# Optimization experiments

Hardware: AMD Instinct MI355X
Metric: run time of the kernel (lower is better)

Reference implementation:

```python
import jax, jax.numpy as jnp
import numpy as np

NQ = 14            # n_qubits
NB = 2             # n_blocks
KLOC = 4           # k_local
K = 2 ** KLOC      # Hermitian observable dim = 16
NOFF = K * (K - 1) // 2   # 120 off-diagonal params
DEPTH = 3          # vqc_depth
IN_DIM = 784
OUT_DIM = 10
BATCH = 128
GROUPS = [list(range(s, s + KLOC)) for s in range(NQ - KLOC + 1)]  # sliding k-local groups
NOBS = len(GROUPS)  # 11
TOTAL_ENC = NB * ((NQ // 2) + ((NQ - 1) // 2)) * 15  # 390 SU(4) encoding params

# 15 two-qubit Pauli words in PennyLane's lexicographic IXYZ order (identity excluded)
_I = np.eye(2, dtype=np.complex64)
_X = np.array([[0, 1], [1, 0]], np.complex64)
_Y = np.array([[0, -1j], [1j, 0]], np.complex64)
_Z = np.array([[1, 0], [0, -1]], np.complex64)
_P = {'I': _I, 'X': _X, 'Y': _Y, 'Z': _Z}
_WORDS = [a + b for a in 'IXYZ' for b in 'IXYZ'][1:]
P15 = jnp.asarray(np.stack([np.kron(_P[w[0]], _P[w[1]]) for w in _WORDS]))  # (15,4,4)
CNOT = jnp.asarray(np.array([[1, 0, 0, 0], [0, 1, 0, 0], [0, 0, 0, 1], [0, 0, 1, 0]], np.complex64))
_ROWS, _COLS = np.tril_indices(K, -1)  # row-major lower-tri order == create_Hermitian fill order


def su4(theta):
    """PennyLane SpecialUnitary: U = expm(i * sum_m theta_m P_m), theta: (B,15).
    The generator is Hermitian, so use eigh instead of generic expm."""
    Hm = jnp.einsum('bm,mij->bij', theta.astype(jnp.complex64), P15)  # (B,4,4) Hermitian
    w, V = jnp.linalg.eigh(Hm)
    return jnp.einsum('bij,bj,bkj->bik', V, jnp.exp(1j * w.astype(jnp.complex64)), V.conj())


def apply_gate(state, U, wires):
    """Apply a k-qubit gate U ((B,2^k,2^k) or (2^k,2^k)) to state (B, 2,...,2)."""
    n = state.ndim - 1
    k = len(wires)
    axes = [w + 1 for w in wires]
    perm = [0] + axes + [a for a in range(1, n + 1) if a not in axes]
    st = jnp.transpose(state, perm)
    shp = st.shape
    st = st.reshape(shp[0], 2 ** k, -1)
    if U.ndim == 3:
        st = jnp.einsum('bij,bjr->bir', U, st)
    else:
        st = jnp.einsum('ij,bjr->bir', U, st)
    return jnp.transpose(st.reshape(shp), np.argsort(perm))


def expval_herm(state, H, wires):
    """<psi| H_{wires} |psi> per batch element."""
    n = state.ndim - 1
    axes = [w + 1 for w in wires]
    perm = [0] + axes + [a for a in range(1, n + 1) if a not in axes]
    st = jnp.transpose(state, perm).reshape(state.shape[0], H.shape[0], -1)
    return jnp.einsum('bkr,kl,blr->b', st.conj(), H, st).real


def create_hermitian(A, Bp, D):
    """Faithful port of create_Hermitian: lower-tri A+iB (row-major), diag D[1:] on
    positions 0..K-2 (D[0] unused, last diag 0), then H = h + h^dagger (diag doubled)."""
    h = jnp.zeros((K, K), jnp.complex64).at[_ROWS, _COLS].set(A + 1j * Bp)
    d = jnp.zeros((K,), A.dtype).at[jnp.arange(K - 1)].set(D[1:])
    h = h + jnp.diag(d).astype(jnp.complex64)
    return h + h.conj().T


def ry_mat(theta):
    c = jnp.cos(theta / 2)
    s = jnp.sin(theta / 2)
    return jnp.stack([jnp.stack([c, -s]), jnp.stack([s, c])]).astype(jnp.complex64)


def setup_inputs():
    key = jax.random.key(0)
    ks = jax.random.split(key, 9)
    lim = 1.0 / np.sqrt(IN_DIM)
    lim_h = 1.0 / np.sqrt(NOBS)
    return {
        'x': jax.random.normal(ks[0], (BATCH, IN_DIM), jnp.float32),
        'W_enc': jax.random.uniform(ks[1], (TOTAL_ENC, IN_DIM), jnp.float32, -lim, lim),
        'b_enc': jax.random.uniform(ks[2], (TOTAL_ENC,), jnp.float32, -lim, lim),
        'var_params': 0.01 * jax.random.normal(ks[3], (DEPTH, NQ), jnp.float32),
        'A': 2.0 * jax.random.normal(ks[4], (NOBS, NOFF), jnp.float32),
        'Bp': 2.0 * jax.random.normal(ks[5], (NOBS, NOFF), jnp.float32),
        'D': 2.0 * jax.random.normal(ks[6], (NOBS, K), jnp.float32),
        'W_head': jax.random.uniform(ks[7], (OUT_DIM, NOBS), jnp.float32, -lim_h, lim_h),
        'b_head': jax.random.uniform(ks[8], (OUT_DIM,), jnp.float32, -lim_h, lim_h),
    }


def reference(x, W_enc, b_enc, var_params, A, Bp, D, W_head, b_head):
    encoded = x @ W_enc.T + b_enc                      # (B, 390)
    Hs = jax.vmap(create_hermitian)(A, Bp, D)          # (NOBS, K, K)
    Bsz = x.shape[0]
    state = jnp.zeros((Bsz,) + (2,) * NQ, jnp.complex64).at[(slice(None),) + (0,) * NQ].set(1.0)
    # SU(4) brick-layer encoding: even pairs then odd pairs per block
    idx = 0
    for _ in range(NB):
        for q in list(range(0, NQ - 1, 2)) + list(range(1, NQ - 1, 2)):
            state = apply_gate(state, su4(encoded[:, idx:idx + 15]), [q, q + 1])
            idx += 15
    # variational RY + CNOT brick layers
    for layer in range(DEPTH):
        for q in range(NQ):
            state = apply_gate(state, ry_mat(var_params[layer, q]), [q])
        for q in list(range(0, NQ - 1, 2)) + list(range(1, NQ - 1, 2)):
            state = apply_gate(state, CNOT, [q, q + 1])
    q_out = jnp.stack([expval_herm(state, Hs[w], GROUPS[w]) for w in range(NOBS)], axis=1)
    q_out = q_out.astype(jnp.float32)                  # (B, NOBS)
    return q_out @ W_head.T + b_head                   # (B, OUT_DIM)
```

## Files before the change

### kernel.cpp

```cpp
#include <hip/hip_runtime.h>
#include <math.h>

#define NQ      14
#define NSTATE  16384
#define BATCH   128
#define DEPTH   3
#define NOBS    11
#define KDIM    16
#define NOFF    120
#define INDIM   784
#define OUTDIM  10

__device__ __forceinline__ int F2(int a) { return a + (a >> 4); }
#define PHYS2 (NSTATE + (NSTATE >> 4))

__device__ __forceinline__ float sbc(float x) {
  return __int_as_float(__builtin_amdgcn_readfirstlane(__float_as_int(x)));
}

__global__ __launch_bounds__(256) void enc_kernel(
    const float* __restrict__ x, const float* __restrict__ W,
    const float* __restrict__ bvec, float* __restrict__ theta)
{
  int wave = ((blockIdx.x << 2) | (threadIdx.x >> 6));
  int lane = threadIdx.x & 63;
  int g = wave >> 7;
  int b = wave & 127;

  const float4* x4 = (const float4*)(x + (size_t)b * INDIM);
  const float4* w4 = (const float4*)(W + (size_t)g * 15 * INDIM);

  float acc[15];
#pragma unroll
  for (int m = 0; m < 15; ++m) acc[m] = 0.f;
#pragma unroll
  for (int it = 0; it < 4; ++it) {
    int j4 = lane + it * 64;
    if (j4 < 196) {
      float4 xv = x4[j4];
#pragma unroll
      for (int m = 0; m < 15; ++m) {
        float4 wv = w4[m * 196 + j4];
        acc[m] = fmaf(xv.x, wv.x, fmaf(xv.y, wv.y, fmaf(xv.z, wv.z, fmaf(xv.w, wv.w, acc[m]))));
      }
    }
  }
#pragma unroll
  for (int m = 0; m < 15; ++m) {
#pragma unroll
    for (int off = 32; off; off >>= 1) acc[m] += __shfl_xor(acc[m], off);
  }
  if (lane == 0) {
#pragma unroll
    for (int m = 0; m < 15; ++m) theta[(size_t)wave * 15 + m] = acc[m] + bvec[g * 15 + m];
  }
}

__global__ __launch_bounds__(256) void expm_kernel(
    const float* __restrict__ theta, float2* __restrict__ Ubuf)
{
  int gid  = blockIdx.x * 256 + threadIdx.x;
  int pair = gid >> 2;
  int j    = gid & 3;
  int lane = threadIdx.x & 63;
  int grp  = lane & 60;

  const float* th = theta + (size_t)pair * 15;

  const float pr_[4][4] = {{1,0,0,1},{0,1,1,0},{0,0,0,0},{1,0,0,-1}};
  const float pi_[4][4] = {{0,0,0,0},{0,0,0,0},{0,-1,1,0},{0,0,0,0}};

  float Hre[16], Him[16];
#pragma unroll
  for (int e = 0; e < 16; ++e) { Hre[e] = 0.f; Him[e] = 0.f; }
  float tsum = 0.f;
#pragma unroll
  for (int m = 0; m < 15; ++m) {
    float tv = th[m];
    tsum += fabsf(tv);
    const int code = m + 1;
    const int a = code >> 2, c = code & 3;
#pragma unroll
    for (int i = 0; i < 4; ++i)
#pragma unroll
      for (int jj = 0; jj < 4; ++jj) {
        float ar = pr_[a][(i >> 1) * 2 + (jj >> 1)], ai = pi_[a][(i >> 1) * 2 + (jj >> 1)];
        float br = pr_[c][(i & 1) * 2 + (jj & 1)],   bi = pi_[c][(i & 1) * 2 + (jj & 1)];
        Hre[i * 4 + jj] += tv * (ar * br - ai * bi);
        Him[i * 4 + jj] += tv * (ar * bi + ai * br);
      }
  }
  int s = 0;
  if (tsum > 0.25f) {
    s = (int)ceilf(log2f(tsum * 4.0f));
    if (s < 0) s = 0;
    if (s > 14) s = 14;
  }
  float sc = exp2f((float)(-s));
  float Gre[16], Gim[16];
#pragma unroll
  for (int e = 0; e < 16; ++e) { Gre[e] = -Him[e] * sc; Gim[e] = Hre[e] * sc; }

  float Tcr[4], Tci[4];
#pragma unroll
  for (int i = 0; i < 4; ++i) {
    Tcr[i] = Gre[i * 4 + j] * (1.f / 9.f) + ((i == j) ? 1.f : 0.f);
    Tci[i] = Gim[i * 4 + j] * (1.f / 9.f);
  }
#pragma unroll
  for (int k = 8; k >= 1; --k) {
    float nr[4], ni[4];
    float invk = 1.0f / (float)k;
#pragma unroll
    for (int i = 0; i < 4; ++i) {
      float xr = 0.f, xi = 0.f;
#pragma unroll
      for (int l = 0; l < 4; ++l) {
        xr = fmaf(Gre[i * 4 + l], Tcr[l], fmaf(-Gim[i * 4 + l], Tci[l], xr));
        xi = fmaf(Gre[i * 4 + l], Tci[l], fmaf( Gim[i * 4 + l], Tcr[l], xi));
      }
      nr[i] = invk * xr + ((i == j) ? 1.f : 0.f);
      ni[i] = invk * xi;
    }
#pragma unroll
    for (int i = 0; i < 4; ++i) { Tcr[i] = nr[i]; Tci[i] = ni[i]; }
  }
  for (int it = 0; it < s; ++it) {
    float nr[4] = {0.f, 0.f, 0.f, 0.f}, ni[4] = {0.f, 0.f, 0.f, 0.f};
#pragma unroll
    for (int l = 0; l < 4; ++l) {
      int src = grp | l;
      float tlr = Tcr[l], tli = Tci[l];
#pragma unroll
      for (int i = 0; i < 4; ++i) {
        float br = __shfl(Tcr[i], src);
        float bi = __shfl(Tci[i], src);
        nr[i] = fmaf(br, tlr, fmaf(-bi, tli, nr[i]));
        ni[i] = fmaf(br, tli, fmaf( bi, tlr, ni[i]));
      }
    }
#pragma unroll
    for (int i = 0; i < 4; ++i) { Tcr[i] = nr[i]; Tci[i] = ni[i]; }
  }
#pragma unroll
  for (int i = 0; i < 4; ++i)
    Ubuf[(size_t)pair * 16 + i * 4 + j] = make_float2(Tcr[i], Tci[i]);
}

template<int S>
__device__ __forceinline__ int grpbase(int t) {
  return ((t >> S) << (S + 4)) | (t & ((1 << S) - 1));
}
template<int S>
__device__ __forceinline__ void ldgrp(const float2* st, int base, float* vr, float* vi) {
#pragma unroll
  for (int k = 0; k < 16; ++k) {
    float2 v = st[F2(base + (k << S))];
    vr[k] = v.x; vi[k] = v.y;
  }
}
template<int S>
__device__ __forceinline__ void stgrp(float2* st, int base, const float* vr, const float* vi) {
#pragma unroll
  for (int k = 0; k < 16; ++k) st[F2(base + (k << S))] = make_float2(vr[k], vi[k]);
}
__device__ __forceinline__ int base2s(int t) {
  return ((t >> 7) << 11) | (((t >> 5) & 3) << 7) | (t & 31);
}
__device__ __forceinline__ int addr2s(int base, int k) {
  return base + ((k >> 2) << 9) + ((k & 3) << 5);
}
__device__ __forceinline__ void ldgrp2(const float2* st, int base, float* vr, float* vi) {
#pragma unroll
  for (int k = 0; k < 16; ++k) {
    float2 v = st[F2(addr2s(base, k))];
    vr[k] = v.x; vi[k] = v.y;
  }
}
__device__ __forceinline__ void stgrp2(float2* st, int base, const float* vr, const float* vi) {
#pragma unroll
  for (int k = 0; k < 16; ++k) st[F2(addr2s(base, k))] = make_float2(vr[k], vi[k]);
}

__device__ __forceinline__ void loadU(const float2* __restrict__ Ug, float* ur, float* ui) {
#pragma unroll
  for (int e = 0; e < 16; ++e) {
    float2 u = Ug[e];
    ur[e] = sbc(u.x); ui[e] = sbc(u.y);
  }
}

__device__ __forceinline__ void applyU_hi(float* vr, float* vi, const float* ur, const float* ui) {
#pragma unroll
  for (int j2 = 0; j2 < 4; ++j2) {
    float ar[4], ai[4];
#pragma unroll
    for (int j = 0; j < 4; ++j) { ar[j] = vr[4 * j + j2]; ai[j] = vi[4 * j + j2]; }
#pragma unroll
    for (int i = 0; i < 4; ++i) {
      float xr = 0.f, xi = 0.f;
#pragma unroll
      for (int j = 0; j < 4; ++j) {
        xr = fmaf(ur[4 * i + j], ar[j], fmaf(-ui[4 * i + j], ai[j], xr));
        xi = fmaf(ur[4 * i + j], ai[j], fmaf( ui[4 * i + j], ar[j], xi));
      }
      vr[4 * i + j2] = xr; vi[4 * i + j2] = xi;
    }
  }
}
__device__ __forceinline__ void applyU_lo(float* vr, float* vi, const float* ur, const float* ui) {
#pragma unroll
  for (int i2 = 0; i2 < 4; ++i2) {
    float ar[4], ai[4];
#pragma unroll
    for (int j = 0; j < 4; ++j) { ar[j] = vr[4 * i2 + j]; ai[j] = vi[4 * i2 + j]; }
#pragma unroll
    for (int i = 0; i < 4; ++i) {
      float xr = 0.f, xi = 0.f;
#pragma unroll
      for (int j = 0; j < 4; ++j) {
        xr = fmaf(ur[4 * i + j], ar[j], fmaf(-ui[4 * i + j], ai[j], xr));
        xi = fmaf(ur[4 * i + j], ai[j], fmaf( ui[4 * i + j], ar[j], xi));
      }
      vr[4 * i2 + i] = xr; vi[4 * i2 + i] = xi;
    }
  }
}
__device__ __forceinline__ void applyU_mid(float* vr, float* vi, const float* ur, const float* ui) {
#pragma unroll
  for (int o = 0; o < 4; ++o) {
    const int kb = ((o >> 1) << 3) | (o & 1);
    float ar[4], ai[4];
#pragma unroll
    for (int j = 0; j < 4; ++j) { ar[j] = vr[kb | (j << 1)]; ai[j] = vi[kb | (j << 1)]; }
#pragma unroll
    for (int i = 0; i < 4; ++i) {
      float xr = 0.f, xi = 0.f;
#pragma unroll
      for (int j = 0; j < 4; ++j) {
        xr = fmaf(ur[4 * i + j], ar[j], fmaf(-ui[4 * i + j], ai[j], xr));
        xi = fmaf(ur[4 * i + j], ai[j], fmaf( ui[4 * i + j], ar[j], xi));
      }
      vr[kb | (i << 1)] = xr; vi[kb | (i << 1)] = xi;
    }
  }
}

template<int B>
__device__ __forceinline__ void ry16(float* vr, float* vi, float c, float s) {
#pragma unroll
  for (int k = 0; k < 16; ++k) {
    if (!(k & (1 << B))) {
      const int k1 = k | (1 << B);
      float r0 = vr[k], i0 = vi[k], r1 = vr[k1], i1 = vi[k1];
      vr[k]  = fmaf(c, r0, -s * r1);  vi[k]  = fmaf(c, i0, -s * i1);
      vr[k1] = fmaf(s, r0,  c * r1);  vi[k1] = fmaf(s, i0,  c * i1);
    }
  }
}
template<int CB, int TB>
__device__ __forceinline__ void cx16(float* vr, float* vi) {
#pragma unroll
  for (int k = 0; k < 16; ++k) {
    if ((k & (1 << CB)) && !(k & (1 << TB))) {
      const int k1 = k | (1 << TB);
      float tr = vr[k]; vr[k] = vr[k1]; vr[k1] = tr;
      float ti = vi[k]; vi[k] = vi[k1]; vi[k1] = ti;
    }
  }
}

template<int S>
__device__ __forceinline__ void enc_pass3(float2* st, const float2* __restrict__ U,
                                          int gHi, int gLo, int gMid, int b, int t) {
  float ur[16], ui[16], vr[16], vi[16];
  int base = grpbase<S>(t);
  ldgrp<S>(st, base, vr, vi);
  loadU(U + ((size_t)gHi  * BATCH + b) * 16, ur, ui); applyU_hi (vr, vi, ur, ui);
  loadU(U + ((size_t)gLo  * BATCH + b) * 16, ur, ui); applyU_lo (vr, vi, ur, ui);
  loadU(U + ((size_t)gMid * BATCH + b) * 16, ur, ui); applyU_mid(vr, vi, ur, ui);
  stgrp<S>(st, base, vr, vi);
}
__device__ __forceinline__ void enc_passD(float2* st, const float2* __restrict__ U,
                                          int gLo, int gMid, int b, int t) {
  float ur[16], ui[16], vr[16], vi[16];
  int base = t << 4;
  ldgrp<0>(st, base, vr, vi);
  loadU(U + ((size_t)gLo  * BATCH + b) * 16, ur, ui); applyU_lo (vr, vi, ur, ui);
  loadU(U + ((size_t)gMid * BATCH + b) * 16, ur, ui); applyU_mid(vr, vi, ur, ui);
  stgrp<0>(st, base, vr, vi);
}
__device__ __forceinline__ void enc_passE(float2* st, const float2* __restrict__ U,
                                          int gA, int gB, int b, int t) {
  float ur[16], ui[16], vr[16], vi[16];
  int base = base2s(t);
  ldgrp2(st, base, vr, vi);
  loadU(U + ((size_t)gA * BATCH + b) * 16, ur, ui); applyU_hi(vr, vi, ur, ui);
  loadU(U + ((size_t)gB * BATCH + b) * 16, ur, ui); applyU_lo(vr, vi, ur, ui);
  stgrp2(st, base, vr, vi);
}
template<int S>
__device__ __forceinline__ void var_pass3(float2* st, const float* __restrict__ vp,
                                          int l, int qbase, int t) {
  float vr[16], vi[16];
  int base = grpbase<S>(t);
  ldgrp<S>(st, base, vr, vi);
  float c[4], sn[4];
#pragma unroll
  for (int i = 0; i < 4; ++i) {
    float a = sbc(vp[l * NQ + qbase + i]) * 0.5f;
    c[i] = cosf(a); sn[i] = sinf(a);
  }
  ry16<3>(vr, vi, c[0], sn[0]);
  ry16<2>(vr, vi, c[1], sn[1]);
  ry16<1>(vr, vi, c[2], sn[2]);
  ry16<0>(vr, vi, c[3], sn[3]);
  cx16<3, 2>(vr, vi);
  cx16<1, 0>(vr, vi);
  cx16<2, 1>(vr, vi);
  stgrp<S>(st, base, vr, vi);
}
__device__ __forceinline__ void var_passD(float2* st, const float* __restrict__ vp,
                                          int l, int t) {
  float vr[16], vi[16];
  int base = t << 4;
  ldgrp<0>(st, base, vr, vi);
  float a0 = sbc(vp[l * NQ + 12]) * 0.5f;
  float a1 = sbc(vp[l * NQ + 13]) * 0.5f;
  ry16<1>(vr, vi, cosf(a0), sinf(a0));
  ry16<0>(vr, vi, cosf(a1), sinf(a1));
  cx16<1, 0>(vr, vi);
  cx16<2, 1>(vr, vi);
  stgrp<0>(st, base, vr, vi);
}
__device__ __forceinline__ void var_passE(float2* st, int t) {
  float vr[16], vi[16];
  int base = base2s(t);
  ldgrp2(st, base, vr, vi);
  cx16<3, 2>(vr, vi);
  cx16<1, 0>(vr, vi);
  stgrp2(st, base, vr, vi);
}

__global__ __launch_bounds__(1024) void qsim_kernel(
    const float2* __restrict__ U, const float* __restrict__ var_params,
    const float* __restrict__ A, const float* __restrict__ Bp,
    const float* __restrict__ D, const float* __restrict__ Wh,
    const float* __restrict__ bh, float* __restrict__ out)
{
  __shared__ float2 st[PHYS2];
  __shared__ float obsa[6 * 256];
  __shared__ float red[6][16];

  const int t = threadIdx.x;
  const int b = blockIdx.x >> 1;
  const int h = blockIdx.x & 1;
  const int nw = h ? 5 : 6;

  for (int i = t; i < PHYS2; i += 1024)
    st[i] = (i == 0) ? make_float2(1.f, 0.f) : make_float2(0.f, 0.f);
  __syncthreads();

  for (int nb = 0; nb < 2; ++nb) {
    int gI = nb * 13;
    enc_pass3<10>(st, U, gI + 0, gI + 1, gI + 7,  b, t); __syncthreads();
    enc_pass3<6 >(st, U, gI + 2, gI + 3, gI + 9,  b, t); __syncthreads();
    enc_pass3<2 >(st, U, gI + 4, gI + 5, gI + 11, b, t); __syncthreads();
    enc_passD    (st, U, gI + 6, gI + 12,         b, t); __syncthreads();
    enc_passE    (st, U, gI + 8, gI + 10,         b, t); __syncthreads();
  }

  for (int l = 0; l < DEPTH; ++l) {
    var_pass3<10>(st, var_params, l, 0, t); __syncthreads();
    var_pass3<6 >(st, var_params, l, 4, t); __syncthreads();
    var_pass3<2 >(st, var_params, l, 8, t); __syncthreads();
    var_passD    (st, var_params, l,    t); __syncthreads();
    var_passE    (st, t);                   __syncthreads();
  }

  for (int i = t; i < nw * 256; i += 1024) {
    int idx = i >> 8, off = i & 255, w = 2 * idx + h;
    float v;
    if (off < NOFF)            v = A[w * NOFF + off];
    else if (off < 2 * NOFF)   v = Bp[w * NOFF + (off - NOFF)];
    else if (off < 2 * NOFF + KDIM) v = D[w * KDIM + (off - 2 * NOFF)];
    else v = 0.f;
    obsa[i] = v;
  }
  __syncthreads();

  const int wave = t >> 6;
  for (int idx = 0; idx < nw; ++idx) {
    const int w = 2 * idx + h;
    const float* ob = &obsa[idx << 8];
    int shift = 10 - w;
    int hi2 = t >> shift;
    int lo = t & ((1 << shift) - 1);
    int base2 = (hi2 << (shift + 4)) | lo;
    float sr[16], si[16];
#pragma unroll
    for (int k = 0; k < 16; ++k) {
      float2 v = st[F2(base2 + (k << shift))];
      sr[k] = v.x; si[k] = v.y;
    }
    float E = 0.f;
#pragma unroll
    for (int k = 0; k < 15; ++k)
      E = fmaf(ob[240 + k + 1], sr[k] * sr[k] + si[k] * si[k], E);
#pragma unroll
    for (int k = 1; k < 16; ++k) {
#pragma unroll
      for (int l2 = 0; l2 < k; ++l2) {
        const int pidx = (k * (k - 1)) / 2 + l2;
        float t1 = sr[k] * sr[l2] + si[k] * si[l2];
        float t2 = si[k] * sr[l2] - sr[k] * si[l2];
        E = fmaf(ob[pidx], t1, fmaf(ob[NOFF + pidx], t2, E));
      }
    }
    E *= 2.0f;
#pragma unroll
    for (int off = 32; off; off >>= 1) E += __shfl_xor(E, off);
    if ((t & 63) == 0) red[idx][wave] = E;
  }
  __syncthreads();

  if (t < OUTDIM) {
    float o = (h == 0) ? bh[t] : 0.f;
    for (int idx = 0; idx < nw; ++idx) {
      const int w = 2 * idx + h;
      float q = 0.f;
#pragma unroll
      for (int ww = 0; ww < 16; ++ww) q += red[idx][ww];
      o = fmaf(Wh[t * NOBS + w], q, o);
    }
    atomicAdd(&out[b * OUTDIM + t], o);
  }
}

extern "C" void kernel_launch(void* const* d_in, const int* in_sizes, int n_in,
                              void* d_out, int out_size, void* d_ws, size_t ws_size,
                              hipStream_t stream) {
  const float* x          = (const float*)d_in[0];
  const float* W_enc      = (const float*)d_in[1];
  const float* b_enc      = (const float*)d_in[2];
  const float* var_params = (const float*)d_in[3];
  const float* A          = (const float*)d_in[4];
  const float* Bp         = (const float*)d_in[5];
  const float* D          = (const float*)d_in[6];
  const float* W_head     = (const float*)d_in[7];
  const float* b_head     = (const float*)d_in[8];
  float* out = (float*)d_out;

  float*  theta = (float*)d_ws;
  size_t  thBytes = (size_t)3328 * 15 * sizeof(float);
  float2* Ubuf = (float2*)((char*)d_ws + ((thBytes + 255) / 256) * 256);

  hipMemsetAsync(out, 0, (size_t)out_size * sizeof(float), stream);
  enc_kernel <<<832, 256, 0, stream>>>(x, W_enc, b_enc, theta);
  expm_kernel<<<52,  256, 0, stream>>>(theta, Ubuf);
  qsim_kernel<<<256, 1024, 0, stream>>>(Ubuf, var_params, A, Bp, D,
                                        W_head, b_head, out);
}
```

Before: 182.1 us.

## Split state simulation and observable evaluation into separate kernels via global state

Before this change, each batch element's 14-qubit state was simulated twice, once in each of two blocks that split the observables between them. Now one block per batch element simulates the state and writes it to a global workspace buffer. A separate kernel then evaluates each observable in its own block, giving 1408 blocks of 256 threads. This removes the duplicated gate simulation and spreads the observable work more widely, at the cost of writing and reading 128 states of 128 KB each through global memory, an extra launch, and only 128 blocks for the gate phase.

```diff
diff --git a/kernel.cpp b/kernel.cpp
--- a/kernel.cpp
+++ b/kernel.cpp
@@ -342,20 +342,14 @@
   stgrp2(st, base, vr, vi);
 }
 
-__global__ __launch_bounds__(1024) void qsim_kernel(
+__global__ __launch_bounds__(1024) void qsim_gates(
     const float2* __restrict__ U, const float* __restrict__ var_params,
-    const float* __restrict__ A, const float* __restrict__ Bp,
-    const float* __restrict__ D, const float* __restrict__ Wh,
-    const float* __restrict__ bh, float* __restrict__ out)
+    float2* __restrict__ gstate)
 {
   __shared__ float2 st[PHYS2];
-  __shared__ float obsa[6 * 256];
-  __shared__ float red[6][16];
 
   const int t = threadIdx.x;
-  const int b = blockIdx.x >> 1;
-  const int h = blockIdx.x & 1;
-  const int nw = h ? 5 : 6;
+  const int b = blockIdx.x;
 
   for (int i = t; i < PHYS2; i += 1024)
     st[i] = (i == 0) ? make_float2(1.f, 0.f) : make_float2(0.f, 0.f);
@@ -378,32 +372,53 @@
     var_passE    (st, t);                   __syncthreads();
   }
 
-  for (int i = t; i < nw * 256; i += 1024) {
-    int idx = i >> 8, off = i & 255, w = 2 * idx + h;
+  float2* gout = gstate + ((size_t)b << 14);
+#pragma unroll
+  for (int j = 0; j < 16; ++j) {
+    int i = t + (j << 10);
+    gout[i] = st[F2(i)];
+  }
+}
+
+__global__ __launch_bounds__(256) void obs_kernel(
+    const float2* __restrict__ gstate,
+    const float* __restrict__ A, const float* __restrict__ Bp,
+    const float* __restrict__ D, const float* __restrict__ Wh,
+    const float* __restrict__ bh, float* __restrict__ out)
+{
+  __shared__ float ob[256];
+  __shared__ float red[4];
+
+  const int t = threadIdx.x;
+  const int w = blockIdx.x >> 7;
+  const int b = blockIdx.x & 127;
+
+  {
     float v;
-    if (off < NOFF)            v = A[w * NOFF + off];
-    else if (off < 2 * NOFF)   v = Bp[w * NOFF + (off - NOFF)];
-    else if (off < 2 * NOFF + KDIM) v = D[w * KDIM + (off - 2 * NOFF)];
-    else v = 0.f;
-    obsa[i] = v;
+    if (t < NOFF)                 v = A[w * NOFF + t];
+    else if (t < 2 * NOFF)        v = Bp[w * NOFF + (t - NOFF)];
+    else                          v = D[w * KDIM + (t - 2 * NOFF)];
+    ob[t] = v;
   }
   __syncthreads();
 
-  const int wave = t >> 6;
-  for (int idx = 0; idx < nw; ++idx) {
-    const int w = 2 * idx + h;
-    const float* ob = &obsa[idx << 8];
-    int shift = 10 - w;
-    int hi2 = t >> shift;
-    int lo = t & ((1 << shift) - 1);
-    int base2 = (hi2 << (shift + 4)) | lo;
+  const float2* stb = gstate + ((size_t)b << 14);
+  const int shift = 10 - w;
+  const int mask = (1 << shift) - 1;
+
+  float E = 0.f;
+#pragma unroll
+  for (int it = 0; it < 4; ++it) {
+    int gg = (it << 8) | t;
+    int hi = gg >> shift;
+    int lo = gg & mask;
+    int base = (hi << (shift + 4)) | lo;
     float sr[16], si[16];
 #pragma unroll
     for (int k = 0; k < 16; ++k) {
-      float2 v = st[F2(base2 + (k << shift))];
+      float2 v = stb[base + (k << shift)];
       sr[k] = v.x; si[k] = v.y;
     }
-    float E = 0.f;
 #pragma unroll
     for (int k = 0; k < 15; ++k)
       E = fmaf(ob[240 + k + 1], sr[k] * sr[k] + si[k] * si[k], E);
@@ -417,22 +432,15 @@
         E = fmaf(ob[pidx], t1, fmaf(ob[NOFF + pidx], t2, E));
       }
     }
-    E *= 2.0f;
-#pragma unroll
-    for (int off = 32; off; off >>= 1) E += __shfl_xor(E, off);
-    if ((t & 63) == 0) red[idx][wave] = E;
-  }
+  }
+#pragma unroll
+  for (int off = 32; off; off >>= 1) E += __shfl_xor(E, off);
+  if ((t & 63) == 0) red[t >> 6] = E;
   __syncthreads();
 
   if (t < OUTDIM) {
-    float o = (h == 0) ? bh[t] : 0.f;
-    for (int idx = 0; idx < nw; ++idx) {
-      const int w = 2 * idx + h;
-      float q = 0.f;
-#pragma unroll
-      for (int ww = 0; ww < 16; ++ww) q += red[idx][ww];
-      o = fmaf(Wh[t * NOBS + w], q, o);
-    }
+    float q = 2.0f * (red[0] + red[1] + red[2] + red[3]);
+    float o = fmaf(Wh[t * NOBS + w], q, (w == 0) ? bh[t] : 0.f);
     atomicAdd(&out[b * OUTDIM + t], o);
   }
 }
@@ -451,13 +459,15 @@
   const float* b_head     = (const float*)d_in[8];
   float* out = (float*)d_out;
 
-  float*  theta = (float*)d_ws;
-  size_t  thBytes = (size_t)3328 * 15 * sizeof(float);
-  float2* Ubuf = (float2*)((char*)d_ws + ((thBytes + 255) / 256) * 256);
+  char* wsb = (char*)d_ws;
+  float*  theta  = (float*)wsb;
+  float2* Ubuf   = (float2*)(wsb + 199680);
+  float2* gstate = (float2*)(wsb + 199680 + 425984);
 
   hipMemsetAsync(out, 0, (size_t)out_size * sizeof(float), stream);
   enc_kernel <<<832, 256, 0, stream>>>(x, W_enc, b_enc, theta);
   expm_kernel<<<52,  256, 0, stream>>>(theta, Ubuf);
-  qsim_kernel<<<256, 1024, 0, stream>>>(Ubuf, var_params, A, Bp, D,
-                                        W_head, b_head, out);
-}
+  qsim_gates <<<128, 1024, 0, stream>>>(Ubuf, var_params, gstate);
+  obs_kernel <<<NOBS * BATCH, 256, 0, stream>>>(gstate, A, Bp, D,
+                                                W_head, b_head, out);
+}
```

Result: slower. 223.2 us (+22.6%).

## Fuse encoder matvec with SU(4) expm and refactor observable expectation

Applied to the files above, without the earlier changes.

Merges the encoder projection kernel and the matrix-exponential kernel into one launch. The first four lanes of each wave now build the 4x4 unitary directly from the reduced theta values, so the theta round trip through global memory and one kernel launch go away. In the simulation kernel, the shared-memory staging of the observable parameters and its barrier are removed. The expectation is rewritten as y = H·psi followed by a dot product, with the Hermitian coefficients read straight from global or constant cache. In exchange, only 4 of 64 lanes do the expm work, and the coefficients are now read per thread from global memory.

```diff
diff --git a/kernel.cpp b/kernel.cpp
--- a/kernel.cpp
+++ b/kernel.cpp
@@ -18,9 +18,9 @@
   return __int_as_float(__builtin_amdgcn_readfirstlane(__float_as_int(x)));
 }
 
-__global__ __launch_bounds__(256) void enc_kernel(
+__global__ __launch_bounds__(256) void enc_expm_kernel(
     const float* __restrict__ x, const float* __restrict__ W,
-    const float* __restrict__ bvec, float* __restrict__ theta)
+    const float* __restrict__ bvec, float2* __restrict__ Ubuf)
 {
   int wave = ((blockIdx.x << 2) | (threadIdx.x >> 6));
   int lane = threadIdx.x & 63;
@@ -50,101 +50,90 @@
 #pragma unroll
     for (int off = 32; off; off >>= 1) acc[m] += __shfl_xor(acc[m], off);
   }
-  if (lane == 0) {
-#pragma unroll
-    for (int m = 0; m < 15; ++m) theta[(size_t)wave * 15 + m] = acc[m] + bvec[g * 15 + m];
-  }
-}
-
-__global__ __launch_bounds__(256) void expm_kernel(
-    const float* __restrict__ theta, float2* __restrict__ Ubuf)
-{
-  int gid  = blockIdx.x * 256 + threadIdx.x;
-  int pair = gid >> 2;
-  int j    = gid & 3;
-  int lane = threadIdx.x & 63;
-  int grp  = lane & 60;
-
-  const float* th = theta + (size_t)pair * 15;
-
-  const float pr_[4][4] = {{1,0,0,1},{0,1,1,0},{0,0,0,0},{1,0,0,-1}};
-  const float pi_[4][4] = {{0,0,0,0},{0,0,0,0},{0,-1,1,0},{0,0,0,0}};
-
-  float Hre[16], Him[16];
-#pragma unroll
-  for (int e = 0; e < 16; ++e) { Hre[e] = 0.f; Him[e] = 0.f; }
-  float tsum = 0.f;
-#pragma unroll
-  for (int m = 0; m < 15; ++m) {
-    float tv = th[m];
-    tsum += fabsf(tv);
-    const int code = m + 1;
-    const int a = code >> 2, c = code & 3;
+
+  if (lane < 4) {
+    const int j = lane;
+    float th[15];
+#pragma unroll
+    for (int m = 0; m < 15; ++m) th[m] = acc[m] + bvec[g * 15 + m];
+
+    const float pr_[4][4] = {{1,0,0,1},{0,1,1,0},{0,0,0,0},{1,0,0,-1}};
+    const float pi_[4][4] = {{0,0,0,0},{0,0,0,0},{0,-1,1,0},{0,0,0,0}};
+    float Hre[16], Him[16];
+#pragma unroll
+    for (int e = 0; e < 16; ++e) { Hre[e] = 0.f; Him[e] = 0.f; }
+    float tsum = 0.f;
+#pragma unroll
+    for (int m = 0; m < 15; ++m) {
+      float tv = th[m];
+      tsum += fabsf(tv);
+      const int code = m + 1;
+      const int a = code >> 2, c = code & 3;
+#pragma unroll
+      for (int i = 0; i < 4; ++i)
+#pragma unroll
+        for (int jj = 0; jj < 4; ++jj) {
+          float ar = pr_[a][(i >> 1) * 2 + (jj >> 1)], ai = pi_[a][(i >> 1) * 2 + (jj >> 1)];
+          float br = pr_[c][(i & 1) * 2 + (jj & 1)],   bi = pi_[c][(i & 1) * 2 + (jj & 1)];
+          Hre[i * 4 + jj] += tv * (ar * br - ai * bi);
+          Him[i * 4 + jj] += tv * (ar * bi + ai * br);
+        }
+    }
+    int s = 0;
+    if (tsum > 0.25f) {
+      s = (int)ceilf(log2f(tsum * 4.0f));
+      if (s < 0) s = 0;
+      if (s > 14) s = 14;
+    }
+    float sc = exp2f((float)(-s));
+    float Gre[16], Gim[16];
+#pragma unroll
+    for (int e = 0; e < 16; ++e) { Gre[e] = -Him[e] * sc; Gim[e] = Hre[e] * sc; }
+
+    float Tcr[4], Tci[4];
+#pragma unroll
+    for (int i = 0; i < 4; ++i) {
+      Tcr[i] = Gre[i * 4 + j] * (1.f / 9.f) + ((i == j) ? 1.f : 0.f);
+      Tci[i] = Gim[i * 4 + j] * (1.f / 9.f);
+    }
+#pragma unroll
+    for (int k = 8; k >= 1; --k) {
+      float nr[4], ni[4];
+      float invk = 1.0f / (float)k;
+#pragma unroll
+      for (int i = 0; i < 4; ++i) {
+        float xr = 0.f, xi = 0.f;
+#pragma unroll
+        for (int l = 0; l < 4; ++l) {
+          xr = fmaf(Gre[i * 4 + l], Tcr[l], fmaf(-Gim[i * 4 + l], Tci[l], xr));
+          xi = fmaf(Gre[i * 4 + l], Tci[l], fmaf( Gim[i * 4 + l], Tcr[l], xi));
+        }
+        nr[i] = invk * xr + ((i == j) ? 1.f : 0.f);
+        ni[i] = invk * xi;
+      }
+#pragma unroll
+      for (int i = 0; i < 4; ++i) { Tcr[i] = nr[i]; Tci[i] = ni[i]; }
+    }
+    for (int it = 0; it < s; ++it) {
+      float nr[4] = {0.f, 0.f, 0.f, 0.f}, ni[4] = {0.f, 0.f, 0.f, 0.f};
+#pragma unroll
+      for (int l = 0; l < 4; ++l) {
+        float tlr = Tcr[l], tli = Tci[l];
+#pragma unroll
+        for (int i = 0; i < 4; ++i) {
+          float br = __shfl(Tcr[i], l);
+          float bi = __shfl(Tci[i], l);
+          nr[i] = fmaf(br, tlr, fmaf(-bi, tli, nr[i]));
+          ni[i] = fmaf(br, tli, fmaf( bi, tlr, ni[i]));
+        }
+      }
+#pragma unroll
+      for (int i = 0; i < 4; ++i) { Tcr[i] = nr[i]; Tci[i] = ni[i]; }
+    }
 #pragma unroll
     for (int i = 0; i < 4; ++i)
-#pragma unroll
-      for (int jj = 0; jj < 4; ++jj) {
-        float ar = pr_[a][(i >> 1) * 2 + (jj >> 1)], ai = pi_[a][(i >> 1) * 2 + (jj >> 1)];
-        float br = pr_[c][(i & 1) * 2 + (jj & 1)],   bi = pi_[c][(i & 1) * 2 + (jj & 1)];
-        Hre[i * 4 + jj] += tv * (ar * br - ai * bi);
-        Him[i * 4 + jj] += tv * (ar * bi + ai * br);
-      }
-  }
-  int s = 0;
-  if (tsum > 0.25f) {
-    s = (int)ceilf(log2f(tsum * 4.0f));
-    if (s < 0) s = 0;
-    if (s > 14) s = 14;
-  }
-  float sc = exp2f((float)(-s));
-  float Gre[16], Gim[16];
-#pragma unroll
-  for (int e = 0; e < 16; ++e) { Gre[e] = -Him[e] * sc; Gim[e] = Hre[e] * sc; }
-
-  float Tcr[4], Tci[4];
-#pragma unroll
-  for (int i = 0; i < 4; ++i) {
-    Tcr[i] = Gre[i * 4 + j] * (1.f / 9.f) + ((i == j) ? 1.f : 0.f);
-    Tci[i] = Gim[i * 4 + j] * (1.f / 9.f);
-  }
-#pragma unroll
-  for (int k = 8; k >= 1; --k) {
-    float nr[4], ni[4];
-    float invk = 1.0f / (float)k;
-#pragma unroll
-    for (int i = 0; i < 4; ++i) {
-      float xr = 0.f, xi = 0.f;
-#pragma unroll
-      for (int l = 0; l < 4; ++l) {
-        xr = fmaf(Gre[i * 4 + l], Tcr[l], fmaf(-Gim[i * 4 + l], Tci[l], xr));
-        xi = fmaf(Gre[i * 4 + l], Tci[l], fmaf( Gim[i * 4 + l], Tcr[l], xi));
-      }
-      nr[i] = invk * xr + ((i == j) ? 1.f : 0.f);
-      ni[i] = invk * xi;
-    }
-#pragma unroll
-    for (int i = 0; i < 4; ++i) { Tcr[i] = nr[i]; Tci[i] = ni[i]; }
-  }
-  for (int it = 0; it < s; ++it) {
-    float nr[4] = {0.f, 0.f, 0.f, 0.f}, ni[4] = {0.f, 0.f, 0.f, 0.f};
-#pragma unroll
-    for (int l = 0; l < 4; ++l) {
-      int src = grp | l;
-      float tlr = Tcr[l], tli = Tci[l];
-#pragma unroll
-      for (int i = 0; i < 4; ++i) {
-        float br = __shfl(Tcr[i], src);
-        float bi = __shfl(Tci[i], src);
-        nr[i] = fmaf(br, tlr, fmaf(-bi, tli, nr[i]));
-        ni[i] = fmaf(br, tli, fmaf( bi, tlr, ni[i]));
-      }
-    }
-#pragma unroll
-    for (int i = 0; i < 4; ++i) { Tcr[i] = nr[i]; Tci[i] = ni[i]; }
-  }
-#pragma unroll
-  for (int i = 0; i < 4; ++i)
-    Ubuf[(size_t)pair * 16 + i * 4 + j] = make_float2(Tcr[i], Tci[i]);
+      Ubuf[(size_t)wave * 16 + i * 4 + j] = make_float2(Tcr[i], Tci[i]);
+  }
 }
 
 template<int S>
@@ -349,7 +338,6 @@
     const float* __restrict__ bh, float* __restrict__ out)
 {
   __shared__ float2 st[PHYS2];
-  __shared__ float obsa[6 * 256];
   __shared__ float red[6][16];
 
   const int t = threadIdx.x;
@@ -378,45 +366,44 @@
     var_passE    (st, t);                   __syncthreads();
   }
 
-  for (int i = t; i < nw * 256; i += 1024) {
-    int idx = i >> 8, off = i & 255, w = 2 * idx + h;
-    float v;
-    if (off < NOFF)            v = A[w * NOFF + off];
-    else if (off < 2 * NOFF)   v = Bp[w * NOFF + (off - NOFF)];
-    else if (off < 2 * NOFF + KDIM) v = D[w * KDIM + (off - 2 * NOFF)];
-    else v = 0.f;
-    obsa[i] = v;
-  }
-  __syncthreads();
-
   const int wave = t >> 6;
   for (int idx = 0; idx < nw; ++idx) {
     const int w = 2 * idx + h;
-    const float* ob = &obsa[idx << 8];
-    int shift = 10 - w;
-    int hi2 = t >> shift;
-    int lo = t & ((1 << shift) - 1);
-    int base2 = (hi2 << (shift + 4)) | lo;
+    const float* __restrict__ Aw = A + w * NOFF;
+    const float* __restrict__ Bw = Bp + w * NOFF;
+    const float* __restrict__ Dw = D + w * KDIM;
+    const int shift = 10 - w;
+    const int hi2 = t >> shift;
+    const int lo = t & ((1 << shift) - 1);
+    const int base2 = (hi2 << (shift + 4)) | lo;
     float sr[16], si[16];
 #pragma unroll
     for (int k = 0; k < 16; ++k) {
       float2 v = st[F2(base2 + (k << shift))];
       sr[k] = v.x; si[k] = v.y;
     }
-    float E = 0.f;
-#pragma unroll
-    for (int k = 0; k < 15; ++k)
-      E = fmaf(ob[240 + k + 1], sr[k] * sr[k] + si[k] * si[k], E);
+    float yr[16], yi[16];
+#pragma unroll
+    for (int k = 0; k < 16; ++k) {
+      float dk = (k < 15) ? Dw[k + 1] : 0.f;
+      yr[k] = dk * sr[k];
+      yi[k] = dk * si[k];
+    }
 #pragma unroll
     for (int k = 1; k < 16; ++k) {
 #pragma unroll
       for (int l2 = 0; l2 < k; ++l2) {
         const int pidx = (k * (k - 1)) / 2 + l2;
-        float t1 = sr[k] * sr[l2] + si[k] * si[l2];
-        float t2 = si[k] * sr[l2] - sr[k] * si[l2];
-        E = fmaf(ob[pidx], t1, fmaf(ob[NOFF + pidx], t2, E));
-      }
-    }
+        const float a = Aw[pidx];
+        const float q = Bw[pidx];
+        yr[k] = fmaf(a, sr[l2], fmaf(-q, si[l2], yr[k]));
+        yi[k] = fmaf(a, si[l2], fmaf( q, sr[l2], yi[k]));
+      }
+    }
+    float E = 0.f;
+#pragma unroll
+    for (int k = 0; k < 16; ++k)
+      E = fmaf(sr[k], yr[k], fmaf(si[k], yi[k], E));
     E *= 2.0f;
 #pragma unroll
     for (int off = 32; off; off >>= 1) E += __shfl_xor(E, off);
@@ -451,13 +438,10 @@
   const float* b_head     = (const float*)d_in[8];
   float* out = (float*)d_out;
 
-  float*  theta = (float*)d_ws;
-  size_t  thBytes = (size_t)3328 * 15 * sizeof(float);
-  float2* Ubuf = (float2*)((char*)d_ws + ((thBytes + 255) / 256) * 256);
+  float2* Ubuf = (float2*)d_ws;
 
   hipMemsetAsync(out, 0, (size_t)out_size * sizeof(float), stream);
-  enc_kernel <<<832, 256, 0, stream>>>(x, W_enc, b_enc, theta);
-  expm_kernel<<<52,  256, 0, stream>>>(theta, Ubuf);
+  enc_expm_kernel<<<832, 256, 0, stream>>>(x, W_enc, b_enc, Ubuf);
   qsim_kernel<<<256, 1024, 0, stream>>>(Ubuf, var_params, A, Bp, D,
                                         W_head, b_head, out);
 }
```

Result: slower. 188.0 us (+3.2%).
